# Kernel tuning notes

Hardware: AMD Instinct MI355X
Metric: run time of the kernel (lower is better)

Reference implementation:

```python
import jax, jax.numpy as jnp
import numpy as np

B, D_MODEL, H = 2048, 1024, 16
D_K = D_MODEL // H


def setup_inputs() -> dict:
    root = jax.random.key(0)
    ks = jax.random.split(root, 11)
    w_scale = 1.0 / np.sqrt(D_MODEL).astype(np.float32)
    inp = {
        "query": jax.random.normal(ks[0], (B, D_MODEL), jnp.float32),
        "key": jax.random.normal(ks[1], (B, D_MODEL), jnp.float32),
        "value": jax.random.normal(ks[2], (B, D_MODEL), jnp.float32),
        # Linear weights (used as x @ W + b)
        "Wq": jax.random.normal(ks[3], (D_MODEL, D_MODEL), jnp.float32) * w_scale,
        "bq": jnp.zeros((D_MODEL,), jnp.float32),
        "Wk": jax.random.normal(ks[4], (D_MODEL, D_MODEL), jnp.float32) * w_scale,
        "bk": jnp.zeros((D_MODEL,), jnp.float32),
        "Wv": jax.random.normal(ks[5], (D_MODEL, D_MODEL), jnp.float32) * w_scale,
        "bv": jnp.zeros((D_MODEL,), jnp.float32),
        # Random U drawn fresh each forward in torch; materialized here for determinism.
        # torch shape: randn(d_model, nbatches*d_k).view(nbatches, h, d_k, d_k)
        "U": jax.random.normal(ks[6], (B, H, D_K, D_K), jnp.float32),
    }
    return inp


def reference(query, key, value, Wq, bq, Wk, bk, Wv, bv, U):
    b, dm = query.shape
    h = U.shape[1]
    dk = dm // h
    residual = key
    # QKV projections, then view(b, -1, h, dk).transpose(1, 2) -> [b, h, 1, dk]
    q = (query @ Wq + bq).reshape(b, 1, h, dk).transpose(0, 2, 1, 3)
    k = (key @ Wk + bk).reshape(b, 1, h, dk).transpose(0, 2, 1, 3)
    v = (value @ Wv + bv).reshape(b, 1, h, dk).transpose(0, 2, 1, 3)
    # attn_weight = (q @ U) @ k^T : [b,h,1,dk] @ [b,h,dk,dk] @ [b,h,dk,1] -> [b,h,1,1]
    aw = jnp.matmul(q, U)
    scores = jnp.matmul(aw, jnp.swapaxes(k, -1, -2))
    p = jax.nn.softmax(scores, axis=-1)  # dropout is identity at inference
    # context = p^T @ v : [b,h,1,1] @ [b,h,1,dk] -> [b,h,1,dk]
    ctx = jnp.matmul(jnp.swapaxes(p, -1, -2), v)
    ctx = jnp.swapaxes(ctx, 1, 2).reshape(b, dm)
    return ctx + residual
```

## Files before the change

kernel.cpp:

```cpp
#include <hip/hip_runtime.h>
#include <hip/hip_bf16.h>


#define M_DIM 2048
#define N_DIM 1024
#define K_DIM 1024

typedef __attribute__((ext_vector_type(8))) short short8;
typedef __attribute__((ext_vector_type(4))) float f32x4;

__device__ inline unsigned rne_bf16(float f) {
    unsigned u = __builtin_bit_cast(unsigned, f);
    return (u + 0x7FFFu + ((u >> 16) & 1u)) >> 16;
}
__device__ inline unsigned pack2(float lo, float hi) {
    return rne_bf16(lo) | (rne_bf16(hi) << 16);
}
__device__ inline void gl_lds16(const short* g, short* l) {
    __builtin_amdgcn_global_load_lds((const __attribute__((address_space(1))) void*)g,
                                     (__attribute__((address_space(3))) void*)l,
                                     16, 0, 0);
}

__global__ __launch_bounds__(256)
void convert_kernel(const float* __restrict__ value, const float* __restrict__ Wv,
                    short* __restrict__ Vb, short* __restrict__ WvTb) {
    __shared__ unsigned tr[64 * 36];
    const int b = blockIdx.x, tid = threadIdx.x;
    if (b < 1024) {
        int g = b * 256 + tid;
        int row = g >> 7, ch = g & 127;
        int kt = ch >> 3, c = ch & 7;
        int tm = row >> 6, r = row & 63;
        const float* p = value + (size_t)row * K_DIM + ch * 8;
        f32x4 a0 = *(const f32x4*)p;
        f32x4 a1 = *(const f32x4*)(p + 4);
        union { short8 s; unsigned u[4]; } o;
        o.u[0] = pack2(a0[0], a0[1]);
        o.u[1] = pack2(a0[2], a0[3]);
        o.u[2] = pack2(a1[0], a1[1]);
        o.u[3] = pack2(a1[2], a1[3]);
        *(short8*)&Vb[(size_t)(tm * 16 + kt) * 4096 + r * 64 + ((c ^ (r & 7)) << 3)] = o.s;
    } else {
        int b2 = b - 1024;
        int tn = b2 & 15, kt = b2 >> 4;
        #pragma unroll
        for (int s = 0; s < 2; ++s) {
            int kp = (tid >> 4) + s * 16;
            int n4 = (tid & 15) * 4;
            const float* bp = Wv + (size_t)(kt * 64 + 2 * kp) * N_DIM + tn * 64 + n4;
            f32x4 b0 = *(const f32x4*)bp;
            f32x4 b1 = *(const f32x4*)(bp + N_DIM);
            #pragma unroll
            for (int m = 0; m < 4; ++m)
                tr[(n4 + m) * 36 + kp] = pack2(b0[m], b1[m]);
        }
        __syncthreads();
        int n = tid >> 2;
        #pragma unroll
        for (int h = 0; h < 2; ++h) {
            int c = (tid & 3) + 4 * h;
            union { short8 s; unsigned u[4]; } o;
            #pragma unroll
            for (int p = 0; p < 4; ++p)
                o.u[p] = tr[n * 36 + c * 4 + p];
            *(short8*)&WvTb[(size_t)(tn * 16 + kt) * 4096 + n * 64 + ((c ^ (n & 7)) << 3)] = o.s;
        }
    }
}

__global__ __launch_bounds__(256)
void gemm_kernel(const short* __restrict__ Vb, const short* __restrict__ WvTb,
                 const float* __restrict__ key, const float* __restrict__ bv,
                 float* __restrict__ out) {
    __shared__ __align__(16) short As[4][8192];
    __shared__ __align__(16) short Bs[4][4096];

    const int tid = threadIdx.x;
    const int bid = blockIdx.x;
    const int xcd = bid & 7, idx = bid >> 3;
    const int bm2 = xcd * 2 + (idx >> 4);
    const int bn  = idx & 15;
    const int lane = tid & 63;
    const int wid = tid >> 6;
    const int wr = wid >> 1;
    const int wc = wid & 1;

    const short* Ab0 = Vb + (size_t)(bm2 * 2) * 16 * 4096;
    const short* Ab1 = Vb + (size_t)(bm2 * 2 + 1) * 16 * 4096;
    const short* Bb  = WvTb + (size_t)bn * 16 * 4096;
    const int row0 = bm2 * 128, col0 = bn * 64;

    const int colA = col0 + wc * 32 + (lane & 15);
    const int rbaseA = row0 + wr * 64 + ((lane >> 4) * 4);
    float keyr[4][2][4];
    float bvr[2];
    #pragma unroll
    for (int fn = 0; fn < 2; ++fn) bvr[fn] = bv[colA + fn * 16];
    #pragma unroll
    for (int fm = 0; fm < 4; ++fm)
        #pragma unroll
        for (int fn = 0; fn < 2; ++fn)
            #pragma unroll
            for (int i = 0; i < 4; ++i)
                keyr[fm][fn][i] = key[(size_t)(rbaseA + fm * 16 + i) * N_DIM + colA + fn * 16];

    f32x4 acc[4][2] = {};

    auto stage = [&](int buf, int kt) {
        const short* ga0 = Ab0 + (size_t)kt * 4096 + tid * 8;
        const short* ga1 = Ab1 + (size_t)kt * 4096 + tid * 8;
        const short* gb  = Bb  + (size_t)kt * 4096 + tid * 8;
        gl_lds16(ga0,        &As[buf][tid * 8]);
        gl_lds16(ga0 + 2048, &As[buf][2048 + tid * 8]);
        gl_lds16(ga1,        &As[buf][4096 + tid * 8]);
        gl_lds16(ga1 + 2048, &As[buf][6144 + tid * 8]);
        gl_lds16(gb,         &Bs[buf][tid * 8]);
        gl_lds16(gb + 2048,  &Bs[buf][2048 + tid * 8]);
    };

    auto compute = [&](int buf) {
        #pragma unroll
        for (int ks = 0; ks < 2; ++ks) {
            short8 afr[4], bfr[2];
            const int g = ks * 4 + (lane >> 4);
            #pragma unroll
            for (int fm = 0; fm < 4; ++fm) {
                int r = fm * 16 + (lane & 15);
                afr[fm] = *(const short8*)&As[buf][wr * 4096 + r * 64 + ((g ^ (r & 7)) << 3)];
            }
            #pragma unroll
            for (int fn = 0; fn < 2; ++fn) {
                int n = wc * 32 + fn * 16 + (lane & 15);
                bfr[fn] = *(const short8*)&Bs[buf][n * 64 + ((g ^ (n & 7)) << 3)];
            }
            #pragma unroll
            for (int fm = 0; fm < 4; ++fm)
                #pragma unroll
                for (int fn = 0; fn < 2; ++fn)
                    acc[fm][fn] = __builtin_amdgcn_mfma_f32_16x16x32_bf16(
                        afr[fm], bfr[fn], acc[fm][fn], 0, 0, 0);
        }
    };

    stage(0, 0);
    stage(1, 1);
    stage(2, 2);

    #pragma unroll
    for (int kt = 0; kt < 16; ++kt) {
        if (kt <= 13)      asm volatile("s_waitcnt vmcnt(12)" ::: "memory");
        else if (kt == 14) asm volatile("s_waitcnt vmcnt(6)" ::: "memory");
        else               asm volatile("s_waitcnt vmcnt(0)" ::: "memory");
        __builtin_amdgcn_s_barrier();
        if (kt + 3 < 16) stage((kt + 3) & 3, kt + 3);
        compute(kt & 3);
    }

    #pragma unroll
    for (int fm = 0; fm < 4; ++fm)
        #pragma unroll
        for (int fn = 0; fn < 2; ++fn) {
            int col = colA + fn * 16;
            #pragma unroll
            for (int i = 0; i < 4; ++i) {
                int r = rbaseA + fm * 16 + i;
                out[(size_t)r * N_DIM + col] = acc[fm][fn][i] + bvr[fn] + keyr[fm][fn][i];
            }
        }
}

extern "C" void kernel_launch(void* const* d_in, const int* in_sizes, int n_in,
                              void* d_out, int out_size, void* d_ws, size_t ws_size,
                              hipStream_t stream) {
    const float* key   = (const float*)d_in[1];
    const float* value = (const float*)d_in[2];
    const float* Wv    = (const float*)d_in[7];
    const float* bv    = (const float*)d_in[8];
    float* out = (float*)d_out;

    short* Vb   = (short*)d_ws;
    short* WvTb = (short*)d_ws + (size_t)M_DIM * K_DIM;

    convert_kernel<<<1024 + 256, 256, 0, stream>>>(value, Wv, Vb, WvTb);
    gemm_kernel<<<256, 256, 0, stream>>>(Vb, WvTb, key, bv, out);
}
```

Before: 26.53 us.

## Split GEMM into 4-way split-K with larger tiles and separate reduction kernel

```diff
diff --git a/kernel.cpp b/kernel.cpp
--- a/kernel.cpp
+++ b/kernel.cpp
@@ -70,59 +70,43 @@
 }
 
 __global__ __launch_bounds__(256)
-void gemm_kernel(const short* __restrict__ Vb, const short* __restrict__ WvTb,
-                 const float* __restrict__ key, const float* __restrict__ bv,
-                 float* __restrict__ out) {
-    __shared__ __align__(16) short As[4][8192];
-    __shared__ __align__(16) short Bs[4][4096];
-
-    const int tid = threadIdx.x;
-    const int bid = blockIdx.x;
+void gemm_splitk(const short* __restrict__ Vb, const short* __restrict__ WvTb,
+                 float* __restrict__ partials) {
+    __shared__ __align__(16) short As[2][8192];
+    __shared__ __align__(16) short Bs[2][8192];
+
+    const int tid = threadIdx.x, bid = blockIdx.x;
     const int xcd = bid & 7, idx = bid >> 3;
-    const int bm2 = xcd * 2 + (idx >> 4);
-    const int bn  = idx & 15;
-    const int lane = tid & 63;
-    const int wid = tid >> 6;
-    const int wr = wid >> 1;
-    const int wc = wid & 1;
-
-    const short* Ab0 = Vb + (size_t)(bm2 * 2) * 16 * 4096;
-    const short* Ab1 = Vb + (size_t)(bm2 * 2 + 1) * 16 * 4096;
-    const short* Bb  = WvTb + (size_t)bn * 16 * 4096;
-    const int row0 = bm2 * 128, col0 = bn * 64;
-
-    const int colA = col0 + wc * 32 + (lane & 15);
-    const int rbaseA = row0 + wr * 64 + ((lane >> 4) * 4);
-    float keyr[4][2][4];
-    float bvr[2];
-    #pragma unroll
-    for (int fn = 0; fn < 2; ++fn) bvr[fn] = bv[colA + fn * 16];
-    #pragma unroll
-    for (int fm = 0; fm < 4; ++fm)
-        #pragma unroll
-        for (int fn = 0; fn < 2; ++fn)
-            #pragma unroll
-            for (int i = 0; i < 4; ++i)
-                keyr[fm][fn][i] = key[(size_t)(rbaseA + fm * 16 + i) * N_DIM + colA + fn * 16];
-
-    f32x4 acc[4][2] = {};
+    const int bm2 = xcd * 2 + (idx >> 5);
+    const int rem = idx & 31;
+    const int bn  = rem >> 2;
+    const int kh  = rem & 3;
+    const int lane = tid & 63, wid = tid >> 6;
+    const int wr = wid >> 1, wc = wid & 1;
+
+    const short* A0 = Vb   + (size_t)(bm2 * 2)     * 16 * 4096;
+    const short* A1 = Vb   + (size_t)(bm2 * 2 + 1) * 16 * 4096;
+    const short* B0 = WvTb + (size_t)(bn * 2)      * 16 * 4096;
+    const short* B1 = WvTb + (size_t)(bn * 2 + 1)  * 16 * 4096;
+
+    f32x4 acc[4][4] = {};
 
     auto stage = [&](int buf, int kt) {
-        const short* ga0 = Ab0 + (size_t)kt * 4096 + tid * 8;
-        const short* ga1 = Ab1 + (size_t)kt * 4096 + tid * 8;
-        const short* gb  = Bb  + (size_t)kt * 4096 + tid * 8;
-        gl_lds16(ga0,        &As[buf][tid * 8]);
-        gl_lds16(ga0 + 2048, &As[buf][2048 + tid * 8]);
-        gl_lds16(ga1,        &As[buf][4096 + tid * 8]);
-        gl_lds16(ga1 + 2048, &As[buf][6144 + tid * 8]);
-        gl_lds16(gb,         &Bs[buf][tid * 8]);
-        gl_lds16(gb + 2048,  &Bs[buf][2048 + tid * 8]);
+        const size_t o = (size_t)kt * 4096 + tid * 8;
+        gl_lds16(A0 + o,        &As[buf][tid * 8]);
+        gl_lds16(A0 + o + 2048, &As[buf][2048 + tid * 8]);
+        gl_lds16(A1 + o,        &As[buf][4096 + tid * 8]);
+        gl_lds16(A1 + o + 2048, &As[buf][6144 + tid * 8]);
+        gl_lds16(B0 + o,        &Bs[buf][tid * 8]);
+        gl_lds16(B0 + o + 2048, &Bs[buf][2048 + tid * 8]);
+        gl_lds16(B1 + o,        &Bs[buf][4096 + tid * 8]);
+        gl_lds16(B1 + o + 2048, &Bs[buf][6144 + tid * 8]);
     };
 
     auto compute = [&](int buf) {
         #pragma unroll
         for (int ks = 0; ks < 2; ++ks) {
-            short8 afr[4], bfr[2];
+            short8 afr[4], bfr[4];
             const int g = ks * 4 + (lane >> 4);
             #pragma unroll
             for (int fm = 0; fm < 4; ++fm) {
@@ -130,44 +114,70 @@
                 afr[fm] = *(const short8*)&As[buf][wr * 4096 + r * 64 + ((g ^ (r & 7)) << 3)];
             }
             #pragma unroll
-            for (int fn = 0; fn < 2; ++fn) {
-                int n = wc * 32 + fn * 16 + (lane & 15);
-                bfr[fn] = *(const short8*)&Bs[buf][n * 64 + ((g ^ (n & 7)) << 3)];
+            for (int fn = 0; fn < 4; ++fn) {
+                int n = fn * 16 + (lane & 15);
+                bfr[fn] = *(const short8*)&Bs[buf][wc * 4096 + n * 64 + ((g ^ (n & 7)) << 3)];
             }
             #pragma unroll
             for (int fm = 0; fm < 4; ++fm)
                 #pragma unroll
-                for (int fn = 0; fn < 2; ++fn)
+                for (int fn = 0; fn < 4; ++fn)
                     acc[fm][fn] = __builtin_amdgcn_mfma_f32_16x16x32_bf16(
                         afr[fm], bfr[fn], acc[fm][fn], 0, 0, 0);
         }
     };
 
-    stage(0, 0);
-    stage(1, 1);
-    stage(2, 2);
-
+    const int k0 = kh * 4;
+    stage(0, k0);
+    stage(1, k0 + 1);
     #pragma unroll
-    for (int kt = 0; kt < 16; ++kt) {
-        if (kt <= 13)      asm volatile("s_waitcnt vmcnt(12)" ::: "memory");
-        else if (kt == 14) asm volatile("s_waitcnt vmcnt(6)" ::: "memory");
-        else               asm volatile("s_waitcnt vmcnt(0)" ::: "memory");
+    for (int kt = 0; kt < 4; ++kt) {
+        if (kt <= 2) asm volatile("s_waitcnt vmcnt(8)" ::: "memory");
+        else         asm volatile("s_waitcnt vmcnt(0)" ::: "memory");
         __builtin_amdgcn_s_barrier();
-        if (kt + 3 < 16) stage((kt + 3) & 3, kt + 3);
-        compute(kt & 3);
+        compute(kt & 1);
+        if (kt + 2 < 4) {
+            __builtin_amdgcn_s_barrier();
+            stage(kt & 1, k0 + kt + 2);
+        }
     }
 
+    float* pk = partials + (size_t)kh * M_DIM * N_DIM;
+    const int row0 = bm2 * 128, col0 = bn * 128;
+    const int colW = col0 + wc * 64 + (lane & 15);
+    const int rowW = row0 + wr * 64 + (lane >> 4) * 4;
     #pragma unroll
     for (int fm = 0; fm < 4; ++fm)
         #pragma unroll
-        for (int fn = 0; fn < 2; ++fn) {
-            int col = colA + fn * 16;
-            #pragma unroll
-            for (int i = 0; i < 4; ++i) {
-                int r = rbaseA + fm * 16 + i;
-                out[(size_t)r * N_DIM + col] = acc[fm][fn][i] + bvr[fn] + keyr[fm][fn][i];
-            }
-        }
+        for (int fn = 0; fn < 4; ++fn) {
+            int col = colW + fn * 16;
+            #pragma unroll
+            for (int i = 0; i < 4; ++i)
+                pk[(size_t)(rowW + fm * 16 + i) * N_DIM + col] = acc[fm][fn][i];
+        }
+}
+
+__global__ __launch_bounds__(256)
+void reduce_kernel(const float* __restrict__ partials, const float* __restrict__ key,
+                   const float* __restrict__ bv, float* __restrict__ out) {
+    const int g = blockIdx.x * 256 + threadIdx.x;
+    const float* p0 = partials;
+    const float* p1 = partials + (size_t)1 * M_DIM * N_DIM;
+    const float* p2 = partials + (size_t)2 * M_DIM * N_DIM;
+    const float* p3 = partials + (size_t)3 * M_DIM * N_DIM;
+    #pragma unroll
+    for (int it = 0; it < 4; ++it) {
+        int q = g + it * 131072;
+        size_t off = (size_t)q * 4;
+        int col4 = (q & 255) * 4;
+        f32x4 s = *(const f32x4*)(p0 + off);
+        s = s + *(const f32x4*)(p1 + off);
+        s = s + *(const f32x4*)(p2 + off);
+        s = s + *(const f32x4*)(p3 + off);
+        s = s + *(const f32x4*)(key + off);
+        s = s + *(const f32x4*)(bv + col4);
+        *(f32x4*)(out + off) = s;
+    }
 }
 
 extern "C" void kernel_launch(void* const* d_in, const int* in_sizes, int n_in,
@@ -179,9 +189,12 @@
     const float* bv    = (const float*)d_in[8];
     float* out = (float*)d_out;
 
-    short* Vb   = (short*)d_ws;
-    short* WvTb = (short*)d_ws + (size_t)M_DIM * K_DIM;
+    char* ws = (char*)d_ws;
+    short* Vb       = (short*)(ws + 0);
+    short* WvTb     = (short*)(ws + (4 << 20));
+    float* partials = (float*)(ws + (8 << 20));
 
     convert_kernel<<<1024 + 256, 256, 0, stream>>>(value, Wv, Vb, WvTb);
-    gemm_kernel<<<256, 256, 0, stream>>>(Vb, WvTb, key, bv, out);
-}
+    gemm_splitk<<<512, 256, 0, stream>>>(Vb, WvTb, partials);
+    reduce_kernel<<<512, 256, 0, stream>>>(partials, key, bv, out);
+}
```

After: 29.77 us. +12.2%, slower.
